# Optimization experiments

Hardware: AMD Instinct MI355X
Metric: run time of the kernel (lower is better)

## Reference

```python
import jax, jax.numpy as jnp
import numpy as np

D_MODEL = 1024
NUM_HEADS = 16
D_K = D_MODEL // NUM_HEADS
NEG = -1e9


def setup_inputs() -> dict:
    key = jax.random.key(0)
    ks = jax.random.split(key, 7)
    B, S = 2, 2048
    q = jax.random.normal(ks[0], (B, S, D_MODEL), dtype=jnp.float32)
    k = jax.random.normal(ks[1], (B, S, D_MODEL), dtype=jnp.float32)
    v = jax.random.normal(ks[2], (B, S, D_MODEL), dtype=jnp.float32)
    mask = jnp.ones((B, S), dtype=jnp.int32)
    # nn.Linear(d_model, d_model, bias=False): y = x @ W.T, W:[out,in]
    scale = 1.0 / np.sqrt(D_MODEL)
    Wq = jax.random.normal(ks[3], (D_MODEL, D_MODEL), dtype=jnp.float32) * scale
    Wk = jax.random.normal(ks[4], (D_MODEL, D_MODEL), dtype=jnp.float32) * scale
    Wv = jax.random.normal(ks[5], (D_MODEL, D_MODEL), dtype=jnp.float32) * scale
    Wo = jax.random.normal(ks[6], (D_MODEL, D_MODEL), dtype=jnp.float32) * scale
    return {"q": q, "k": k, "v": v, "mask": mask,
            "Wq": Wq, "Wk": Wk, "Wv": Wv, "Wo": Wo}


def _split_heads(x, B):
    # [B,S,D] -> [B,H,S,d_k]
    return x.reshape(B, -1, NUM_HEADS, D_K).transpose(0, 2, 1, 3)


def reference(q, k, v, mask, Wq, Wk, Wv, Wo):
    B = q.shape[0]
    qh = _split_heads(q @ Wq.T, B)
    kh = _split_heads(k @ Wk.T, B)
    vh = _split_heads(v @ Wv.T, B)
    # [B,H,Sq,Sk]
    scores = jnp.einsum('bhqd,bhkd->bhqk', qh, kh) / jnp.sqrt(jnp.float32(D_K))
    Sq, Sk = scores.shape[-2], scores.shape[-1]
    causal = jnp.triu(jnp.ones((Sq, Sk), dtype=bool), k=1)
    scores = jnp.where(causal[None, None], NEG, scores)
    pad = (mask[:, None, None, :] == 0)  # [B,1,1,Sk]
    scores = jnp.where(pad, NEG, scores)
    weights = jax.nn.softmax(scores, axis=-1)
    out = jnp.einsum('bhqk,bhkd->bhqd', weights, vh)
    out = out.transpose(0, 2, 1, 3).reshape(B, -1, D_MODEL)
    return out @ Wo.T
```

## Files before the change

### kernel.cpp

```cpp
#include <hip/hip_runtime.h>
#include <hip/hip_bf16.h>
#include <stdint.h>

using bf16 = __hip_bfloat16;
typedef __attribute__((ext_vector_type(8))) short short8;
typedef __attribute__((ext_vector_type(4))) float f32x4;
typedef __attribute__((ext_vector_type(16))) float f32x16;
typedef __attribute__((ext_vector_type(4))) float float4v;
typedef __attribute__((ext_vector_type(4))) unsigned short us4;
typedef __attribute__((ext_vector_type(4))) uint32_t u32x4;

#define LDS_U32 __attribute__((address_space(3))) uint32_t
#define GLB_U32 __attribute__((address_space(1))) uint32_t

__device__ __forceinline__ unsigned short f2b(float f) {
  union { float f; uint32_t u; } x; x.f = f;
  uint32_t r = x.u + 0x7FFFu + ((x.u >> 16) & 1u);
  return (unsigned short)(r >> 16);
}

__global__ void cast_multi(const float* __restrict__ s0, const float* __restrict__ s1,
                           const float* __restrict__ s2, const float* __restrict__ s3,
                           bf16* __restrict__ d0, bf16* __restrict__ d1,
                           bf16* __restrict__ d2, bf16* __restrict__ d3,
                           int nvec, int narr) {
  int total = nvec * narr;
  for (int i = blockIdx.x * blockDim.x + threadIdx.x; i < total;
       i += gridDim.x * blockDim.x) {
    int a = i / nvec, vi = i - a * nvec;
    const float* s = (a == 0) ? s0 : (a == 1) ? s1 : (a == 2) ? s2 : s3;
    bf16* d = (a == 0) ? d0 : (a == 1) ? d1 : (a == 2) ? d2 : d3;
    float4v x = ((const float4v*)s)[vi];
    us4 y;
    y.x = f2b(x.x); y.y = f2b(x.y); y.z = f2b(x.z); y.w = f2b(x.w);
    ((us4*)d)[vi] = y;
  }
}

__global__ __launch_bounds__(256, 2)
void qkv_proj(const bf16* __restrict__ Aq, const bf16* __restrict__ Ak,
              const bf16* __restrict__ Av,
              const bf16* __restrict__ Wq, const bf16* __restrict__ Wk,
              const bf16* __restrict__ Wv,
              bf16* __restrict__ Qh, bf16* __restrict__ Kh, bf16* __restrict__ Vt) {
  __shared__ bf16 Alds[128 * 64];
  __shared__ bf16 Blds[128 * 64];
  const int t = threadIdx.x, lane = t & 63, wave = t >> 6;
  const int l15 = lane & 15, l4 = lane >> 4;
  const int seg = blockIdx.x >> 3;
  const int n0 = (blockIdx.x & 7) * 128;
  const int m0 = blockIdx.y * 128;
  const bf16* A = (seg == 0) ? Aq : (seg == 1) ? Ak : Av;
  const bf16* B = (seg == 0) ? Wq : (seg == 1) ? Wk : Wv;
  const int K = 1024;
  const int wr = (wave >> 1) * 64, wc = (wave & 1) * 64;

  f32x4 acc[4][4] = {};

  for (int kt = 0; kt < K; kt += 64) {
#pragma unroll
    for (int i = 0; i < 4; ++i) {
      int f = i * 256 + t, row = f >> 3, csrc = (f & 7) ^ (row & 7);
      __builtin_amdgcn_global_load_lds(
          (const GLB_U32*)(A + (size_t)(m0 + row) * K + kt + csrc * 8),
          (LDS_U32*)(Alds + f * 8), 16, 0, 0);
      __builtin_amdgcn_global_load_lds(
          (const GLB_U32*)(B + (size_t)(n0 + row) * K + kt + csrc * 8),
          (LDS_U32*)(Blds + f * 8), 16, 0, 0);
    }
    __syncthreads();
#pragma unroll
    for (int ks = 0; ks < 2; ++ks) {
      short8 af[4], bfr[4];
#pragma unroll
      for (int mi = 0; mi < 4; ++mi) {
        int row = wr + mi * 16 + l15;
        int ch = (ks * 4 + l4) ^ (row & 7);
        af[mi] = *(const short8*)(Alds + row * 64 + ch * 8);
      }
#pragma unroll
      for (int ni = 0; ni < 4; ++ni) {
        int row = wc + ni * 16 + l15;
        int ch = (ks * 4 + l4) ^ (row & 7);
        bfr[ni] = *(const short8*)(Blds + row * 64 + ch * 8);
      }
#pragma unroll
      for (int mi = 0; mi < 4; ++mi)
#pragma unroll
        for (int ni = 0; ni < 4; ++ni)
          acc[mi][ni] = __builtin_amdgcn_mfma_f32_16x16x32_bf16(
              af[mi], bfr[ni], acc[mi][ni], 0, 0, 0);
    }
    __syncthreads();
  }

#pragma unroll
  for (int mi = 0; mi < 4; ++mi) {
#pragma unroll
    for (int ni = 0; ni < 4; ++ni) {
      int rbase = m0 + wr + mi * 16 + l4 * 4;
      int col = n0 + wc + ni * 16 + l15;
      if (seg < 2) {
        unsigned short* C = (unsigned short*)((seg == 0) ? Qh : Kh);
#pragma unroll
        for (int r = 0; r < 4; ++r)
          C[(size_t)(rbase + r) * 1024 + col] = f2b(acc[mi][ni][r]);
      } else {
        unsigned short* C = (unsigned short*)Vt;
        int bb = rbase >> 11, sidx = rbase & 2047;
        size_t addr = ((size_t)(bb * 1024 + col)) * 2048 + sidx;
        us4 y;
        y.x = f2b(acc[mi][ni][0]); y.y = f2b(acc[mi][ni][1]);
        y.z = f2b(acc[mi][ni][2]); y.w = f2b(acc[mi][ni][3]);
        *(us4*)(C + addr) = y;
      }
    }
  }
}

__global__ __launch_bounds__(256, 2)
void gemm_o(const bf16* __restrict__ A, const bf16* __restrict__ B,
            float* __restrict__ C) {
  __shared__ bf16 Alds[128 * 64];
  __shared__ bf16 Blds[64 * 64];
  const int t = threadIdx.x, lane = t & 63, wave = t >> 6;
  const int l15 = lane & 15, l4 = lane >> 4;
  const int n0 = blockIdx.x * 64, m0 = blockIdx.y * 128;
  const int K = 1024;
  const int wr = (wave >> 1) * 64, wc = (wave & 1) * 32;

  f32x4 acc[4][2] = {};

  for (int kt = 0; kt < K; kt += 64) {
#pragma unroll
    for (int i = 0; i < 4; ++i) {
      int f = i * 256 + t, row = f >> 3, csrc = (f & 7) ^ (row & 7);
      __builtin_amdgcn_global_load_lds(
          (const GLB_U32*)(A + (size_t)(m0 + row) * K + kt + csrc * 8),
          (LDS_U32*)(Alds + f * 8), 16, 0, 0);
    }
#pragma unroll
    for (int i = 0; i < 2; ++i) {
      int f = i * 256 + t, row = f >> 3, csrc = (f & 7) ^ (row & 7);
      __builtin_amdgcn_global_load_lds(
          (const GLB_U32*)(B + (size_t)(n0 + row) * K + kt + csrc * 8),
          (LDS_U32*)(Blds + f * 8), 16, 0, 0);
    }
    __syncthreads();
#pragma unroll
    for (int ks = 0; ks < 2; ++ks) {
      short8 af[4], bfr[2];
#pragma unroll
      for (int mi = 0; mi < 4; ++mi) {
        int row = wr + mi * 16 + l15;
        int ch = (ks * 4 + l4) ^ (row & 7);
        af[mi] = *(const short8*)(Alds + row * 64 + ch * 8);
      }
#pragma unroll
      for (int ni = 0; ni < 2; ++ni) {
        int row = wc + ni * 16 + l15;
        int ch = (ks * 4 + l4) ^ (row & 7);
        bfr[ni] = *(const short8*)(Blds + row * 64 + ch * 8);
      }
#pragma unroll
      for (int mi = 0; mi < 4; ++mi)
#pragma unroll
        for (int ni = 0; ni < 2; ++ni)
          acc[mi][ni] = __builtin_amdgcn_mfma_f32_16x16x32_bf16(
              af[mi], bfr[ni], acc[mi][ni], 0, 0, 0);
    }
    __syncthreads();
  }

#pragma unroll
  for (int mi = 0; mi < 4; ++mi)
#pragma unroll
    for (int ni = 0; ni < 2; ++ni) {
      int rbase = m0 + wr + mi * 16 + l4 * 4;
      int col = n0 + wc + ni * 16 + l15;
#pragma unroll
      for (int r = 0; r < 4; ++r)
        C[(size_t)(rbase + r) * 1024 + col] = acc[mi][ni][r];
    }
}

__global__ __launch_bounds__(256, 2)
void attn_fwd(const bf16* __restrict__ Q, const bf16* __restrict__ K,
              const bf16* __restrict__ Vt, const int* __restrict__ mask,
              bf16* __restrict__ O) {
  const int lin = blockIdx.x;
  const int xcd = lin & 7, q8 = lin >> 3;
  const int bh = xcd + 8 * (q8 & 3), g = q8 >> 2;
  const int b = bh >> 4, h = bh & 15;
  const int wave = threadIdx.x >> 6, lane = threadIdx.x & 63;
  const int l31 = lane & 31, hi = lane >> 5;
  const int job = 2 * g + (wave >> 1);
  const int halfk = wave & 1, wp = wave >> 1;

  __shared__ float accL[2][64][33];
  __shared__ float mlL[2][64][2];

  const size_t bqk = (size_t)b * 2048 * 1024 + h * 64;
  const size_t vbase = ((size_t)b * 1024 + h * 64) * 2048;
  const float SCLE = 0.18033688011112042f;

  for (int si = 0; si < 2; ++si) {
    const int s = si ? (63 - job) : job;
    const int q0 = 32 * s;
    const int T = (s >> 1) + 1;
    const int hsplit = (T + 1) >> 1;
    const int tstart = halfk ? hsplit : 0;
    const int tend = halfk ? T : hsplit;

    short8 qf[4];
#pragma unroll
    for (int s4 = 0; s4 < 4; ++s4)
      qf[s4] = *(const short8*)(Q + bqk + (size_t)(q0 + l31) * 1024 + 16 * s4 + 8 * hi);

    f32x16 acc0 = {}, acc1 = {};
    float m = -1e30f, l = 0.f;

    short8 kf[2][4], kn[2][4], vf[2][4];
    if (tstart < tend) {
#pragma unroll
      for (int u = 0; u < 2; ++u)
#pragma unroll
        for (int s4 = 0; s4 < 4; ++s4)
          kf[u][s4] = *(const short8*)(K + bqk +
              (size_t)(tstart * 64 + 32 * u + l31) * 1024 + 16 * s4 + 8 * hi);
    }

    for (int tt = tstart; tt < tend; ++tt) {
#pragma unroll
      for (int n = 0; n < 2; ++n)
#pragma unroll
        for (int t = 0; t < 4; ++t)
          vf[n][t] = *(const short8*)(Vt + vbase + (size_t)(32 * n + l31) * 2048 +
                                      tt * 64 + 16 * t + 8 * hi);
      int mv = mask[b * 2048 + tt * 64 + lane];

      f32x16 s0 = {}, s1 = {};
#pragma unroll
      for (int s4 = 0; s4 < 4; ++s4) {
        s0 = __builtin_amdgcn_mfma_f32_32x32x16_bf16(kf[0][s4], qf[s4], s0, 0, 0, 0);
        s1 = __builtin_amdgcn_mfma_f32_32x32x16_bf16(kf[1][s4], qf[s4], s1, 0, 0, 0);
      }
      if (tt + 1 < tend) {
#pragma unroll
        for (int u = 0; u < 2; ++u)
#pragma unroll
          for (int s4 = 0; s4 < 4; ++s4)
            kn[u][s4] = *(const short8*)(K + bqk +
                (size_t)((tt + 1) * 64 + 32 * u + l31) * 1024 + 16 * s4 + 8 * hi);
      }

      float w[2][16];
#pragma unroll
      for (int p = 0; p < 16; ++p) { w[0][p] = s0[p] * SCLE; w[1][p] = s1[p] * SCLE; }

      uint64_t bits = __ballot(mv != 0);
      if (bits != ~0ull) {
        uint64_t bs = bits >> (4 * hi);
#pragma unroll
        for (int u = 0; u < 2; ++u)
#pragma unroll
          for (int p = 0; p < 16; ++p)
            if (!((bs >> (32 * u + (p & 3) + 8 * (p >> 2))) & 1)) w[u][p] = -3e38f;
      }
      if (tt == T - 1) {
        int qr = 32 * (s & 1) + l31 - 4 * hi;
#pragma unroll
        for (int u = 0; u < 2; ++u)
#pragma unroll
          for (int p = 0; p < 16; ++p)
            if (32 * u + (p & 3) + 8 * (p >> 2) > qr) w[u][p] = -3e38f;
      }

      float tm = fmaxf(w[0][0], w[1][0]);
#pragma unroll
      for (int p = 1; p < 16; ++p) tm = fmaxf(tm, fmaxf(w[0][p], w[1][p]));
      tm = fmaxf(tm, __shfl_xor(tm, 32));

      if (!__all(tm <= m + 8.f)) {
        float mn = fmaxf(m, tm);
        float corr = __builtin_amdgcn_exp2f(m - mn);
        m = mn; l *= corr;
#pragma unroll
        for (int p = 0; p < 16; ++p) {
          float ct = __shfl(corr, (p & 3) + 8 * (p >> 2) + 4 * hi);
          acc0[p] *= ct; acc1[p] *= ct;
        }
      }

      float ts = 0.f;
#pragma unroll
      for (int u = 0; u < 2; ++u)
#pragma unroll
        for (int p = 0; p < 16; ++p) {
          float pv = __builtin_amdgcn_exp2f(w[u][p] - m);
          w[u][p] = pv; ts += pv;
        }
      ts += __shfl_xor(ts, 32);
      l += ts;

      uint32_t pkk[2][8];
#pragma unroll
      for (int u = 0; u < 2; ++u)
#pragma unroll
        for (int a = 0; a < 4; ++a)
#pragma unroll
          for (int w2 = 0; w2 < 2; ++w2) {
            uint32_t r;
            asm("v_cvt_pk_bf16_f32 %0, %1, %2"
                : "=v"(r) : "v"(w[u][4 * a + 2 * w2]), "v"(w[u][4 * a + 2 * w2 + 1]));
            pkk[u][2 * a + w2] = r;
          }

#pragma unroll
      for (int t = 0; t < 4; ++t) {
        const int u = t >> 1, alo = 2 * (t & 1);
        uint32_t wd[4];
#pragma unroll
        for (int w2 = 0; w2 < 2; ++w2) {
          uint32_t own_lo = pkk[u][2 * alo + w2];
          uint32_t own_hi = pkk[u][2 * alo + 2 + w2];
          uint32_t pre = hi ? own_lo : own_hi;
          uint32_t sx = (uint32_t)__shfl_xor((int)pre, 32);
          wd[w2] = hi ? sx : own_lo;
          wd[2 + w2] = hi ? own_hi : sx;
        }
        u32x4 wv = {wd[0], wd[1], wd[2], wd[3]};
        short8 paf = __builtin_bit_cast(short8, wv);
        acc0 = __builtin_amdgcn_mfma_f32_32x32x16_bf16(paf, vf[0][t], acc0, 0, 0, 0);
        acc1 = __builtin_amdgcn_mfma_f32_32x32x16_bf16(paf, vf[1][t], acc1, 0, 0, 0);
      }

#pragma unroll
      for (int u = 0; u < 2; ++u)
#pragma unroll
        for (int s4 = 0; s4 < 4; ++s4) kf[u][s4] = kn[u][s4];
    }

    if (halfk) {
#pragma unroll
      for (int p = 0; p < 16; ++p) {
        accL[wp][lane][p] = acc0[p];
        accL[wp][lane][16 + p] = acc1[p];
      }
      mlL[wp][lane][0] = m; mlL[wp][lane][1] = l;
    }
    __syncthreads();
    if (!halfk) {
      float mB = mlL[wp][lane][0], lB = mlL[wp][lane][1];
      float ms = fmaxf(m, mB);
      float cAr = __builtin_amdgcn_exp2f(m - ms);
      float cBr = __builtin_amdgcn_exp2f(mB - ms);
      float inv = 1.f / (cAr * l + cBr * lB);
      float fa = cAr * inv, fb = cBr * inv;
      unsigned short* Ou = (unsigned short*)O;
#pragma unroll
      for (int p = 0; p < 16; ++p) {
        int crow = (p & 3) + 8 * (p >> 2) + 4 * hi;
        float faT = __shfl(fa, crow);
        float fbT = __shfl(fb, crow);
        float o0 = acc0[p] * faT + accL[wp][lane][p] * fbT;
        float o1 = acc1[p] * faT + accL[wp][lane][16 + p] * fbT;
        size_t ro = (size_t)(b * 2048 + q0 + crow) * 1024 + h * 64;
        Ou[ro + l31] = f2b(o0);
        Ou[ro + 32 + l31] = f2b(o1);
      }
    }
    __syncthreads();
  }
}

extern "C" void kernel_launch(void* const* d_in, const int* in_sizes, int n_in,
                              void* d_out, int out_size, void* d_ws, size_t ws_size,
                              hipStream_t stream) {
  const float* q = (const float*)d_in[0];
  const float* k = (const float*)d_in[1];
  const float* v = (const float*)d_in[2];
  const int* mask = (const int*)d_in[3];
  const float* Wq = (const float*)d_in[4];
  const float* Wk = (const float*)d_in[5];
  const float* Wv = (const float*)d_in[6];
  const float* Wo = (const float*)d_in[7];
  float* out = (float*)d_out;

  const size_t NT = 4096 * 1024;
  const size_t NW = 1024 * 1024;
  bf16* p = (bf16*)d_ws;
  bf16* qb = p;  p += NT;
  bf16* kb = p;  p += NT;
  bf16* vb = p;  p += NT;
  bf16* Wqb = p; p += NW;
  bf16* Wkb = p; p += NW;
  bf16* Wvb = p; p += NW;
  bf16* Wob = p; p += NW;
  bf16* Qh = p;  p += NT;
  bf16* Kh = p;  p += NT;
  bf16* Vt = p;  p += NT;
  bf16* Oh = p;  p += NT;

  cast_multi<<<2048, 256, 0, stream>>>(q, k, v, nullptr, qb, kb, vb, nullptr,
                                       (int)(NT / 4), 3);
  cast_multi<<<1024, 256, 0, stream>>>(Wq, Wk, Wv, Wo, Wqb, Wkb, Wvb, Wob,
                                       (int)(NW / 4), 4);
  qkv_proj<<<dim3(24, 32), 256, 0, stream>>>(qb, kb, vb, Wqb, Wkb, Wvb, Qh, Kh, Vt);
  attn_fwd<<<512, 256, 0, stream>>>(Qh, Kh, Vt, mask, Oh);
  gemm_o<<<dim3(16, 32), 256, 0, stream>>>(Oh, Wob, out);
}
```

Before: 233.2 us.

## Fuse fp32-to-bf16 casts into GEMM staging and pre-swizzle K/V for attention

Removes the two standalone cast kernels and converts fp32 inputs and weights to bf16 while staging them into LDS inside the projection and output GEMMs. The softmax scale is folded into the Q projection epilogue. K and V are written in fragment-ordered layouts so the attention kernel can issue contiguous loads. The attention kernel also checks the mask once per query block and skips per-tile ballots when no padding is present, replaces the shuffle-based P repack with v_permlane32_swap, and raises wave priority around the MFMAs. The cost is that the GEMMs now read fp32 through registers instead of direct global-to-LDS loads, doubling their input bytes and losing async LDS fills.

```diff
diff --git a/kernel.cpp b/kernel.cpp
--- a/kernel.cpp
+++ b/kernel.cpp
@@ -19,30 +19,24 @@
   return (unsigned short)(r >> 16);
 }
 
-__global__ void cast_multi(const float* __restrict__ s0, const float* __restrict__ s1,
-                           const float* __restrict__ s2, const float* __restrict__ s3,
-                           bf16* __restrict__ d0, bf16* __restrict__ d1,
-                           bf16* __restrict__ d2, bf16* __restrict__ d3,
-                           int nvec, int narr) {
-  int total = nvec * narr;
-  for (int i = blockIdx.x * blockDim.x + threadIdx.x; i < total;
-       i += gridDim.x * blockDim.x) {
-    int a = i / nvec, vi = i - a * nvec;
-    const float* s = (a == 0) ? s0 : (a == 1) ? s1 : (a == 2) ? s2 : s3;
-    bf16* d = (a == 0) ? d0 : (a == 1) ? d1 : (a == 2) ? d2 : d3;
-    float4v x = ((const float4v*)s)[vi];
-    us4 y;
-    y.x = f2b(x.x); y.y = f2b(x.y); y.z = f2b(x.z); y.w = f2b(x.w);
-    ((us4*)d)[vi] = y;
-  }
+__device__ __forceinline__ void stage8(const float* __restrict__ src, bf16* dst) {
+  float4v x0 = *(const float4v*)src;
+  float4v x1 = *(const float4v*)(src + 4);
+  uint32_t p0, p1, p2, p3;
+  asm("v_cvt_pk_bf16_f32 %0, %1, %2" : "=v"(p0) : "v"(x0.x), "v"(x0.y));
+  asm("v_cvt_pk_bf16_f32 %0, %1, %2" : "=v"(p1) : "v"(x0.z), "v"(x0.w));
+  asm("v_cvt_pk_bf16_f32 %0, %1, %2" : "=v"(p2) : "v"(x1.x), "v"(x1.y));
+  asm("v_cvt_pk_bf16_f32 %0, %1, %2" : "=v"(p3) : "v"(x1.z), "v"(x1.w));
+  u32x4 w = {p0, p1, p2, p3};
+  *(u32x4*)dst = w;
 }
 
 __global__ __launch_bounds__(256, 2)
-void qkv_proj(const bf16* __restrict__ Aq, const bf16* __restrict__ Ak,
-              const bf16* __restrict__ Av,
-              const bf16* __restrict__ Wq, const bf16* __restrict__ Wk,
-              const bf16* __restrict__ Wv,
-              bf16* __restrict__ Qh, bf16* __restrict__ Kh, bf16* __restrict__ Vt) {
+void qkv_proj(const float* __restrict__ Aq, const float* __restrict__ Ak,
+              const float* __restrict__ Av,
+              const float* __restrict__ Wq, const float* __restrict__ Wk,
+              const float* __restrict__ Wv,
+              bf16* __restrict__ Qh, bf16* __restrict__ KF, bf16* __restrict__ VF) {
   __shared__ bf16 Alds[128 * 64];
   __shared__ bf16 Blds[128 * 64];
   const int t = threadIdx.x, lane = t & 63, wave = t >> 6;
@@ -50,23 +44,20 @@
   const int seg = blockIdx.x >> 3;
   const int n0 = (blockIdx.x & 7) * 128;
   const int m0 = blockIdx.y * 128;
-  const bf16* A = (seg == 0) ? Aq : (seg == 1) ? Ak : Av;
-  const bf16* B = (seg == 0) ? Wq : (seg == 1) ? Wk : Wv;
+  const float* A = (seg == 0) ? Aq : (seg == 1) ? Ak : Av;
+  const float* B = (seg == 0) ? Wq : (seg == 1) ? Wk : Wv;
   const int K = 1024;
   const int wr = (wave >> 1) * 64, wc = (wave & 1) * 64;
+  const float SCLE = 0.18033688011112042f;
 
   f32x4 acc[4][4] = {};
 
   for (int kt = 0; kt < K; kt += 64) {
 #pragma unroll
     for (int i = 0; i < 4; ++i) {
-      int f = i * 256 + t, row = f >> 3, csrc = (f & 7) ^ (row & 7);
-      __builtin_amdgcn_global_load_lds(
-          (const GLB_U32*)(A + (size_t)(m0 + row) * K + kt + csrc * 8),
-          (LDS_U32*)(Alds + f * 8), 16, 0, 0);
-      __builtin_amdgcn_global_load_lds(
-          (const GLB_U32*)(B + (size_t)(n0 + row) * K + kt + csrc * 8),
-          (LDS_U32*)(Blds + f * 8), 16, 0, 0);
+      int f = i * 256 + t, row = f >> 3, cc = f & 7, ch = cc ^ (row & 7);
+      stage8(A + (size_t)(m0 + row) * K + kt + cc * 8, Alds + row * 64 + ch * 8);
+      stage8(B + (size_t)(n0 + row) * K + kt + cc * 8, Blds + row * 64 + ch * 8);
     }
     __syncthreads();
 #pragma unroll
@@ -100,26 +91,43 @@
     for (int ni = 0; ni < 4; ++ni) {
       int rbase = m0 + wr + mi * 16 + l4 * 4;
       int col = n0 + wc + ni * 16 + l15;
-      if (seg < 2) {
-        unsigned short* C = (unsigned short*)((seg == 0) ? Qh : Kh);
+      if (seg == 0) {
+        unsigned short* C = (unsigned short*)Qh;
 #pragma unroll
         for (int r = 0; r < 4; ++r)
-          C[(size_t)(rbase + r) * 1024 + col] = f2b(acc[mi][ni][r]);
+          C[(size_t)(rbase + r) * 1024 + col] = f2b(acc[mi][ni][r] * SCLE);
+      } else if (seg == 1) {
+        unsigned short* C = (unsigned short*)KF;
+        int h = col >> 6, d = col & 63;
+#pragma unroll
+        for (int r = 0; r < 4; ++r) {
+          int row = rbase + r;
+          int b = row >> 11, s = row & 2047;
+          size_t idx = (size_t)(b * 16 + h) * 131072 +
+                       ((((s >> 5) * 4 + (d >> 4)) * 2 + ((d >> 3) & 1)) * 256) +
+                       (s & 31) * 8 + (d & 7);
+          C[idx] = f2b(acc[mi][ni][r]);
+        }
       } else {
-        unsigned short* C = (unsigned short*)Vt;
-        int bb = rbase >> 11, sidx = rbase & 2047;
-        size_t addr = ((size_t)(bb * 1024 + col)) * 2048 + sidx;
+        unsigned short* C = (unsigned short*)VF;
+        int h = col >> 6, d = col & 63;
+        int row = rbase;
+        int b = row >> 11, s = row & 2047;
+        size_t idx = (size_t)(b * 16 + h) * 131072 +
+                     (((((s >> 6) * 2 + ((d >> 5) & 1)) * 4 + ((s >> 4) & 3)) * 2 +
+                       ((s >> 3) & 1)) * 256) +
+                     (d & 31) * 8 + (s & 7);
         us4 y;
         y.x = f2b(acc[mi][ni][0]); y.y = f2b(acc[mi][ni][1]);
         y.z = f2b(acc[mi][ni][2]); y.w = f2b(acc[mi][ni][3]);
-        *(us4*)(C + addr) = y;
+        *(us4*)(C + idx) = y;
       }
     }
   }
 }
 
 __global__ __launch_bounds__(256, 2)
-void gemm_o(const bf16* __restrict__ A, const bf16* __restrict__ B,
+void gemm_o(const bf16* __restrict__ A, const float* __restrict__ B,
             float* __restrict__ C) {
   __shared__ bf16 Alds[128 * 64];
   __shared__ bf16 Blds[64 * 64];
@@ -141,10 +149,8 @@
     }
 #pragma unroll
     for (int i = 0; i < 2; ++i) {
-      int f = i * 256 + t, row = f >> 3, csrc = (f & 7) ^ (row & 7);
-      __builtin_amdgcn_global_load_lds(
-          (const GLB_U32*)(B + (size_t)(n0 + row) * K + kt + csrc * 8),
-          (LDS_U32*)(Blds + f * 8), 16, 0, 0);
+      int f = i * 256 + t, row = f >> 3, cc = f & 7, ch = cc ^ (row & 7);
+      stage8(B + (size_t)(n0 + row) * K + kt + cc * 8, Blds + row * 64 + ch * 8);
     }
     __syncthreads();
 #pragma unroll
@@ -185,8 +191,8 @@
 }
 
 __global__ __launch_bounds__(256, 2)
-void attn_fwd(const bf16* __restrict__ Q, const bf16* __restrict__ K,
-              const bf16* __restrict__ Vt, const int* __restrict__ mask,
+void attn_fwd(const bf16* __restrict__ Q, const bf16* __restrict__ KF,
+              const bf16* __restrict__ VF, const int* __restrict__ mask,
               bf16* __restrict__ O) {
   const int lin = blockIdx.x;
   const int xcd = lin & 7, q8 = lin >> 3;
@@ -201,8 +207,7 @@
   __shared__ float mlL[2][64][2];
 
   const size_t bqk = (size_t)b * 2048 * 1024 + h * 64;
-  const size_t vbase = ((size_t)b * 1024 + h * 64) * 2048;
-  const float SCLE = 0.18033688011112042f;
+  const size_t fbase = (size_t)bh * 131072;
 
   for (int si = 0; si < 2; ++si) {
     const int s = si ? (63 - job) : job;
@@ -217,6 +222,11 @@
     for (int s4 = 0; s4 < 4; ++s4)
       qf[s4] = *(const short8*)(Q + bqk + (size_t)(q0 + l31) * 1024 + 16 * s4 + 8 * hi);
 
+    int anyz = 0;
+    for (int i = tstart * 64 + lane; i < tend * 64; i += 64)
+      anyz |= (mask[b * 2048 + i] == 0);
+    const bool doMask = __any(anyz);
+
     f32x16 acc0 = {}, acc1 = {};
     float m = -1e30f, l = 0.f;
 
@@ -226,40 +236,42 @@
       for (int u = 0; u < 2; ++u)
 #pragma unroll
         for (int s4 = 0; s4 < 4; ++s4)
-          kf[u][s4] = *(const short8*)(K + bqk +
-              (size_t)(tstart * 64 + 32 * u + l31) * 1024 + 16 * s4 + 8 * hi);
+          kf[u][s4] = *(const short8*)(KF + fbase +
+              ((size_t)((2 * tstart + u) * 4 + s4) * 2 + hi) * 256 + l31 * 8);
     }
 
     for (int tt = tstart; tt < tend; ++tt) {
 #pragma unroll
       for (int n = 0; n < 2; ++n)
 #pragma unroll
-        for (int t = 0; t < 4; ++t)
-          vf[n][t] = *(const short8*)(Vt + vbase + (size_t)(32 * n + l31) * 2048 +
-                                      tt * 64 + 16 * t + 8 * hi);
-      int mv = mask[b * 2048 + tt * 64 + lane];
+        for (int tq = 0; tq < 4; ++tq)
+          vf[n][tq] = *(const short8*)(VF + fbase +
+              ((size_t)(((tt * 2 + n) * 4 + tq) * 2 + hi)) * 256 + l31 * 8);
 
       f32x16 s0 = {}, s1 = {};
+      __builtin_amdgcn_s_setprio(1);
 #pragma unroll
       for (int s4 = 0; s4 < 4; ++s4) {
         s0 = __builtin_amdgcn_mfma_f32_32x32x16_bf16(kf[0][s4], qf[s4], s0, 0, 0, 0);
         s1 = __builtin_amdgcn_mfma_f32_32x32x16_bf16(kf[1][s4], qf[s4], s1, 0, 0, 0);
       }
+      __builtin_amdgcn_s_setprio(0);
       if (tt + 1 < tend) {
 #pragma unroll
         for (int u = 0; u < 2; ++u)
 #pragma unroll
           for (int s4 = 0; s4 < 4; ++s4)
-            kn[u][s4] = *(const short8*)(K + bqk +
-                (size_t)((tt + 1) * 64 + 32 * u + l31) * 1024 + 16 * s4 + 8 * hi);
+            kn[u][s4] = *(const short8*)(KF + fbase +
+                ((size_t)((2 * (tt + 1) + u) * 4 + s4) * 2 + hi) * 256 + l31 * 8);
       }
 
       float w[2][16];
 #pragma unroll
-      for (int p = 0; p < 16; ++p) { w[0][p] = s0[p] * SCLE; w[1][p] = s1[p] * SCLE; }
-
-      uint64_t bits = __ballot(mv != 0);
-      if (bits != ~0ull) {
+      for (int p = 0; p < 16; ++p) { w[0][p] = s0[p]; w[1][p] = s1[p]; }
+
+      if (doMask) {
+        int mv = mask[b * 2048 + tt * 64 + lane];
+        uint64_t bits = __ballot(mv != 0);
         uint64_t bs = bits >> (4 * hi);
 #pragma unroll
         for (int u = 0; u < 2; ++u)
@@ -317,22 +329,18 @@
           }
 
 #pragma unroll
-      for (int t = 0; t < 4; ++t) {
-        const int u = t >> 1, alo = 2 * (t & 1);
-        uint32_t wd[4];
-#pragma unroll
-        for (int w2 = 0; w2 < 2; ++w2) {
-          uint32_t own_lo = pkk[u][2 * alo + w2];
-          uint32_t own_hi = pkk[u][2 * alo + 2 + w2];
-          uint32_t pre = hi ? own_lo : own_hi;
-          uint32_t sx = (uint32_t)__shfl_xor((int)pre, 32);
-          wd[w2] = hi ? sx : own_lo;
-          wd[2 + w2] = hi ? own_hi : sx;
-        }
-        u32x4 wv = {wd[0], wd[1], wd[2], wd[3]};
+      for (int tq = 0; tq < 4; ++tq) {
+        const int u = tq >> 1, alo = 2 * (tq & 1);
+        uint32_t a0 = pkk[u][2 * alo + 0], b0 = pkk[u][2 * alo + 2];
+        uint32_t a1 = pkk[u][2 * alo + 1], b1 = pkk[u][2 * alo + 3];
+        asm("v_permlane32_swap_b32 %0, %1" : "+v"(a0), "+v"(b0));
+        asm("v_permlane32_swap_b32 %0, %1" : "+v"(a1), "+v"(b1));
+        u32x4 wv = {a0, a1, b0, b1};
         short8 paf = __builtin_bit_cast(short8, wv);
-        acc0 = __builtin_amdgcn_mfma_f32_32x32x16_bf16(paf, vf[0][t], acc0, 0, 0, 0);
-        acc1 = __builtin_amdgcn_mfma_f32_32x32x16_bf16(paf, vf[1][t], acc1, 0, 0, 0);
+        __builtin_amdgcn_s_setprio(1);
+        acc0 = __builtin_amdgcn_mfma_f32_32x32x16_bf16(paf, vf[0][tq], acc0, 0, 0, 0);
+        acc1 = __builtin_amdgcn_mfma_f32_32x32x16_bf16(paf, vf[1][tq], acc1, 0, 0, 0);
+        __builtin_amdgcn_s_setprio(0);
       }
 
 #pragma unroll
@@ -388,25 +396,13 @@
   float* out = (float*)d_out;
 
   const size_t NT = 4096 * 1024;
-  const size_t NW = 1024 * 1024;
   bf16* p = (bf16*)d_ws;
-  bf16* qb = p;  p += NT;
-  bf16* kb = p;  p += NT;
-  bf16* vb = p;  p += NT;
-  bf16* Wqb = p; p += NW;
-  bf16* Wkb = p; p += NW;
-  bf16* Wvb = p; p += NW;
-  bf16* Wob = p; p += NW;
-  bf16* Qh = p;  p += NT;
-  bf16* Kh = p;  p += NT;
-  bf16* Vt = p;  p += NT;
-  bf16* Oh = p;  p += NT;
-
-  cast_multi<<<2048, 256, 0, stream>>>(q, k, v, nullptr, qb, kb, vb, nullptr,
-                                       (int)(NT / 4), 3);
-  cast_multi<<<1024, 256, 0, stream>>>(Wq, Wk, Wv, Wo, Wqb, Wkb, Wvb, Wob,
-                                       (int)(NW / 4), 4);
-  qkv_proj<<<dim3(24, 32), 256, 0, stream>>>(qb, kb, vb, Wqb, Wkb, Wvb, Qh, Kh, Vt);
-  attn_fwd<<<512, 256, 0, stream>>>(Qh, Kh, Vt, mask, Oh);
-  gemm_o<<<dim3(16, 32), 256, 0, stream>>>(Oh, Wob, out);
-}
+  bf16* Qh = p; p += NT;
+  bf16* KF = p; p += NT;
+  bf16* VF = p; p += NT;
+  bf16* Oh = p; p += NT;
+
+  qkv_proj<<<dim3(24, 32), 256, 0, stream>>>(q, k, v, Wq, Wk, Wv, Qh, KF, VF);
+  attn_fwd<<<512, 256, 0, stream>>>(Qh, KF, VF, mask, Oh);
+  gemm_o<<<dim3(16, 32), 256, 0, stream>>>(Oh, Wo, out);
+}
```

Result: faster. 223.9 us (-4.0%).
